# Kernel tuning notes

Hardware: AMD Instinct MI355X
Metric: run time of the kernel (lower is better)

## Reference

```python
import jax, jax.numpy as jnp
import numpy as np


def _ternarize(p, delta, w):
    # {-w, 0, +w} via threshold mask, matching TrainableTernarize.forward
    return jnp.where(p > delta, w, jnp.where(p < -delta, -w, jnp.zeros_like(p)))


def _ternary_para(p, w):
    # TrainableTernaryPara.forward: delta = 0.05 * max|p|
    delta = 0.05 * jnp.max(jnp.abs(p))
    return _ternarize(p, delta, w)


def _init_scale(p):
    # w init: mean(|p|[|p| > 0.7 * mean|p|])
    a = jnp.abs(p)
    mask = (a > 0.7 * jnp.mean(a)).astype(p.dtype)
    return jnp.sum(a * mask) / jnp.sum(mask)


def setup_inputs() -> dict:
    key = jax.random.key(0)
    k1, k2, k3 = jax.random.split(key, 3)
    B, S, D_IN, D_OUT = 4, 2048, 4096, 4096
    x = jax.random.normal(k1, (B, S, D_IN), dtype=jnp.float32)
    bound = 1.0 / np.sqrt(D_IN)  # nn.Linear default init range
    W = jax.random.uniform(k2, (D_OUT, D_IN), minval=-bound, maxval=bound, dtype=jnp.float32)
    b = jax.random.uniform(k3, (D_OUT,), minval=-bound, maxval=bound, dtype=jnp.float32)
    w_scale = _init_scale(W)
    b_scale = _init_scale(b)
    return {"x": x, "W": W, "w_scale": w_scale, "b": b, "b_scale": b_scale}


def reference(x, W, w_scale, b, b_scale):
    Wt = _ternary_para(W, w_scale)   # [D_OUT, D_IN] in {-w,0,+w}
    bt = _ternary_para(b, b_scale)   # [D_OUT]
    # F.linear(x, Wt, bt) = x @ Wt.T + bt
    return jnp.einsum('bsi,oi->bso', x, Wt) + bt
```

## Files before the change

kernel.cpp:

```cpp
#include <hip/hip_runtime.h>

typedef int v4i __attribute__((ext_vector_type(4)));
typedef int v16i __attribute__((ext_vector_type(16)));

#define BM 256
#define BN 256
#define BKB 64
#define NRING 4

#define GLOAD_LDS(gptr, lptr)                                                         \
  __builtin_amdgcn_global_load_lds(                                                   \
      (const __attribute__((address_space(1))) unsigned int*)(gptr),                  \
      (__attribute__((address_space(3))) unsigned int*)(lptr), 16, 0, 0)


__device__ __forceinline__ float max4abs(float4 v) {
  return fmaxf(fmaxf(fabsf(v.x), fabsf(v.y)), fmaxf(fabsf(v.z), fabsf(v.w)));
}

__device__ __forceinline__ int packq4(float4 v, float inv) {
  int b0 = ((int)fminf(127.f, fmaxf(-127.f, rintf(v.x * inv)))) & 255;
  int b1 = ((int)fminf(127.f, fmaxf(-127.f, rintf(v.y * inv)))) & 255;
  int b2 = ((int)fminf(127.f, fmaxf(-127.f, rintf(v.z * inv)))) & 255;
  int b3 = ((int)fminf(127.f, fmaxf(-127.f, rintf(v.w * inv)))) & 255;
  return b0 | (b1 << 8) | (b2 << 16) | (b3 << 24);
}

__global__ void prep1_kernel(const float4* __restrict__ X4,
                             signed char* __restrict__ Q,
                             float* __restrict__ sx, int K, int nrows,
                             const float4* __restrict__ W4, long nW4,
                             const float4* __restrict__ b4, int nb4,
                             unsigned* __restrict__ mx) {
  __shared__ float sm[4];
  const int tid = threadIdx.x;
  const int bid = blockIdx.x;

  if (bid < nrows) {
    const float4* xr = X4 + (size_t)bid * (K / 4);
    float4 v0 = xr[tid], v1 = xr[tid + 256], v2 = xr[tid + 512], v3 = xr[tid + 768];
    float m = fmaxf(fmaxf(max4abs(v0), max4abs(v1)), fmaxf(max4abs(v2), max4abs(v3)));
    for (int off = 32; off > 0; off >>= 1) m = fmaxf(m, __shfl_down(m, off));
    if ((tid & 63) == 0) sm[tid >> 6] = m;
    __syncthreads();
    const float total = fmaxf(fmaxf(sm[0], sm[1]), fmaxf(sm[2], sm[3]));
    const float inv = 127.f / total;
    int* qw = (int*)(Q + (size_t)bid * K);
    qw[tid]       = packq4(v0, inv);
    qw[tid + 256] = packq4(v1, inv);
    qw[tid + 512] = packq4(v2, inv);
    qw[tid + 768] = packq4(v3, inv);
    if (tid == 0) sx[bid] = total * (1.f / 127.f);
    return;
  }

  float m = 0.f;
  const bool isB = (bid == gridDim.x - 1);
  if (!isB) {
    const long wb = bid - nrows;
    const long stride = 1024L * blockDim.x;
    for (long i = wb * blockDim.x + tid; i < nW4; i += stride)
      m = fmaxf(m, max4abs(W4[i]));
  } else {
    for (int i = tid; i < nb4; i += blockDim.x) m = fmaxf(m, max4abs(b4[i]));
  }
  for (int off = 32; off > 0; off >>= 1) m = fmaxf(m, __shfl_down(m, off));
  if ((tid & 63) == 0) sm[tid >> 6] = m;
  __syncthreads();
  if (tid == 0) {
    m = fmaxf(fmaxf(sm[0], sm[1]), fmaxf(sm[2], sm[3]));
    atomicMax(mx + (isB ? 1 : 0), __float_as_uint(m));
  }
}

__global__ void prep_w_kernel(const float4* __restrict__ W4, long nW4,
                              const float4* __restrict__ b4, int nb4,
                              const unsigned* __restrict__ mx,
                              const float* __restrict__ bscale,
                              int* __restrict__ Twi, float4* __restrict__ bt) {
  if (blockIdx.x == gridDim.x - 1) {
    const float delta = 0.05f * __uint_as_float(mx[1]);
    const float s = *bscale;
    for (int i = threadIdx.x; i < nb4; i += blockDim.x) {
      float4 v = b4[i];
      float4 o;
      o.x = v.x > delta ? s : (v.x < -delta ? -s : 0.f);
      o.y = v.y > delta ? s : (v.y < -delta ? -s : 0.f);
      o.z = v.z > delta ? s : (v.z < -delta ? -s : 0.f);
      o.w = v.w > delta ? s : (v.w < -delta ? -s : 0.f);
      bt[i] = o;
    }
    return;
  }
  const float delta = 0.05f * __uint_as_float(mx[0]);
  const long stride = (long)(gridDim.x - 1) * blockDim.x;
  for (long i = blockIdx.x * (long)blockDim.x + threadIdx.x; i < nW4; i += stride) {
    float4 w = W4[i];
    int b0 = w.x > delta ? 1 : (w.x < -delta ? 0xFF : 0);
    int b1 = w.y > delta ? 1 : (w.y < -delta ? 0xFF : 0);
    int b2 = w.z > delta ? 1 : (w.z < -delta ? 0xFF : 0);
    int b3 = w.w > delta ? 1 : (w.w < -delta ? 0xFF : 0);
    Twi[i] = b0 | (b1 << 8) | (b2 << 16) | (b3 << 24);
  }
}

__global__ __launch_bounds__(512, 2) void gemm_tern_i8(
    const signed char* __restrict__ A,
    const signed char* __restrict__ B,
    const float* __restrict__ sx,
    const float* __restrict__ bt,
    const float* __restrict__ wsc,
    float* __restrict__ C,
    int M, int N, int K) {
  __shared__ __align__(16) signed char lds[NRING][2][BM * BKB];

  const int tid = threadIdx.x;
  const int wave = tid >> 6;
  const int lane = tid & 63;
  const int wm = wave >> 2, wn = wave & 3;
  const int l32 = lane & 31;
  const int khalf = lane >> 5;

  const unsigned orig = blockIdx.x;
  const unsigned xcd = orig & 7;
  const unsigned r8 = orig >> 3;
  const int by = (int)(xcd * 4 + (r8 & 3));
  const int bx = (int)(r8 >> 2);
  const int bm0 = by * BM;
  const int bn0 = bx * BN;

  const signed char* gA[2];
  const signed char* gB[2];
#pragma unroll
  for (int j = 0; j < 2; ++j) {
    const int idx = j * 512 + tid;
    const int row = idx >> 2;
    const int gch = (idx & 3) ^ ((idx >> 3) & 3);
    gA[j] = A + (size_t)(bm0 + row) * K + gch * 16;
    gB[j] = B + (size_t)(bn0 + row) * K + gch * 16;
  }
  const int ldsbase = wave * 64 * 16;

#define STAGE(slot)                                  \
  do {                                               \
    signed char* la = &lds[slot][0][ldsbase];        \
    signed char* lb = &lds[slot][1][ldsbase];        \
    GLOAD_LDS(gA[0], la);                            \
    GLOAD_LDS(gA[1], la + 8192);                     \
    GLOAD_LDS(gB[0], lb);                            \
    GLOAD_LDS(gB[1], lb + 8192);                     \
    gA[0] += BKB; gA[1] += BKB;                      \
    gB[0] += BKB; gB[1] += BKB;                      \
  } while (0)

  const int q = (l32 >> 1) & 3;
  const int pos0 = (khalf + 0) ^ q;
  const int pos1 = (khalf + 2) ^ q;
  const int aoff0 = (wm * 128 + l32) * BKB + pos0 * 16;
  const int aoff1 = (wm * 128 + l32) * BKB + pos1 * 16;
  const int boff0 = (wn * 64 + l32) * BKB + pos0 * 16;
  const int boff1 = (wn * 64 + l32) * BKB + pos1 * 16;

  v16i acc[4][2] = {};
  v4i bfA[2][2], bfB[2][2];

  const int NT = K / BKB;

  STAGE(0); STAGE(1); STAGE(2);
  asm volatile("s_waitcnt vmcnt(4)" ::: "memory");
  asm volatile("s_barrier" ::: "memory");

#pragma unroll
  for (int nt = 0; nt < 2; ++nt) {
    bfA[nt][0] = *(const v4i*)(&lds[0][1][0] + boff0 + nt * 2048);
    bfA[nt][1] = *(const v4i*)(&lds[0][1][0] + boff1 + nt * 2048);
  }

#define BODY(T, CUR, NXT)                                                              \
  do {                                                                                 \
    const int slot_ = (T) & 3;                                                         \
    if ((T) + 3 < NT) STAGE(((T) + 3) & 3);                                            \
    const signed char* sa_ = &lds[slot_][0][0];                                        \
    v4i af_[4][2];                                                                     \
    _Pragma("unroll")                                                                  \
    for (int mt = 0; mt < 4; ++mt) {                                                   \
      af_[mt][0] = *(const v4i*)(sa_ + aoff0 + mt * 2048);                             \
      af_[mt][1] = *(const v4i*)(sa_ + aoff1 + mt * 2048);                             \
    }                                                                                  \
    if ((T) + 1 < NT) {                                                                \
      const signed char* sbn_ = &lds[((T) + 1) & 3][1][0];                             \
      _Pragma("unroll")                                                                \
      for (int nt = 0; nt < 2; ++nt) {                                                 \
        NXT[nt][0] = *(const v4i*)(sbn_ + boff0 + nt * 2048);                          \
        NXT[nt][1] = *(const v4i*)(sbn_ + boff1 + nt * 2048);                          \
      }                                                                                \
    }                                                                                  \
    __builtin_amdgcn_s_setprio(1);                                                     \
    _Pragma("unroll")                                                                  \
    for (int mt = 0; mt < 4; ++mt)                                                     \
      _Pragma("unroll")                                                                \
      for (int nt = 0; nt < 2; ++nt) {                                                 \
        acc[mt][nt] = __builtin_amdgcn_mfma_i32_32x32x32_i8(af_[mt][0], CUR[nt][0],    \
                                                            acc[mt][nt], 0, 0, 0);    \
        acc[mt][nt] = __builtin_amdgcn_mfma_i32_32x32x32_i8(af_[mt][1], CUR[nt][1],    \
                                                            acc[mt][nt], 0, 0, 0);    \
      }                                                                                \
    __builtin_amdgcn_s_setprio(0);                                                     \
    asm volatile("s_waitcnt vmcnt(4)" ::: "memory");                                   \
    asm volatile("s_barrier" ::: "memory");                                            \
  } while (0)

  for (int t = 0; t < NT - 2; t += 2) {
    BODY(t, bfA, bfB);
    BODY(t + 1, bfB, bfA);
  }
  asm volatile("s_waitcnt vmcnt(0)" ::: "memory");
  asm volatile("s_barrier" ::: "memory");
  BODY(NT - 2, bfA, bfB);
  BODY(NT - 1, bfB, bfA);
#undef BODY
#undef STAGE

  const float ws = *wsc;
#pragma unroll
  for (int mt = 0; mt < 4; ++mt) {
    const int rowbase = bm0 + wm * 128 + mt * 32 + 4 * khalf;
#pragma unroll
    for (int nt = 0; nt < 2; ++nt) {
      const int col = bn0 + wn * 64 + nt * 32 + l32;
      const float bias = bt[col];
#pragma unroll
      for (int r = 0; r < 16; ++r) {
        const int row = rowbase + (r & 3) + 8 * (r >> 2);
        C[(size_t)row * N + col] = ws * sx[row] * (float)acc[mt][nt][r] + bias;
      }
    }
  }
}


extern "C" void kernel_launch(void* const* d_in, const int* in_sizes, int n_in,
                              void* d_out, int out_size, void* d_ws, size_t ws_size,
                              hipStream_t stream) {
  const float* x = (const float*)d_in[0];
  const float* W = (const float*)d_in[1];
  const float* w_scale = (const float*)d_in[2];
  const float* b = (const float*)d_in[3];
  const float* b_scale = (const float*)d_in[4];
  float* out = (float*)d_out;

  const int K = 4096;
  const int N = in_sizes[3];
  const int M = in_sizes[0] / K;

  char* ws = (char*)d_ws;
  signed char* xb = (signed char*)ws;
  signed char* Tw = (signed char*)(ws + (size_t)M * K);
  float* bt = (float*)(ws + (size_t)M * K + (size_t)N * K);
  float* sx = bt + N;
  unsigned* mx = (unsigned*)(sx + M);

  hipMemsetAsync(mx, 0, 8, stream);

  const long nW4 = (long)N * K / 4;
  const int nb4 = N / 4;

  prep1_kernel<<<M + 1024 + 1, 256, 0, stream>>>((const float4*)x, xb, sx, K, M,
                                                 (const float4*)W, nW4,
                                                 (const float4*)b, nb4, mx);

  prep_w_kernel<<<2049, 256, 0, stream>>>((const float4*)W, nW4,
                                          (const float4*)b, nb4, mx, b_scale,
                                          (int*)Tw, (float4*)bt);

  const int nwg = (N / BN) * (M / BM);
  gemm_tern_i8<<<nwg, 512, 0, stream>>>(xb, Tw, sx, bt, w_scale, out, M, N, K);
}
```

Measured before the change: 413.1 us.

## Shrink GEMM tile to 256x128 with 4 waves and 3-slot LDS ring

Changes the int8 GEMM block tile from 256x256 with 8 waves to 256x128 with 4 waves. The LDS ring drops from 4 to 3 stages, packed into one flat buffer, and the LDS swizzle is adjusted. The B-fragment prefetch across iterations is removed, so each step loads A and B fragments from the current slot. The intent is a smaller LDS footprint and more workgroups for better occupancy and load balance, at the cost of lower arithmetic intensity per tile and less latency hiding from the register double-buffering.

```diff
diff --git a/kernel.cpp b/kernel.cpp
--- a/kernel.cpp
+++ b/kernel.cpp
@@ -4,9 +4,10 @@
 typedef int v16i __attribute__((ext_vector_type(16)));
 
 #define BM 256
-#define BN 256
+#define BN 128
 #define BKB 64
-#define NRING 4
+#define SLOT (BM * BKB + BN * BKB)
+#define NRING 3
 
 #define GLOAD_LDS(gptr, lptr)                                                         \
   __builtin_amdgcn_global_load_lds(                                                   \
@@ -104,7 +105,7 @@
   }
 }
 
-__global__ __launch_bounds__(512, 2) void gemm_tern_i8(
+__global__ __launch_bounds__(256, 2) void gemm_tern_i8(
     const signed char* __restrict__ A,
     const signed char* __restrict__ B,
     const float* __restrict__ sx,
@@ -112,12 +113,12 @@
     const float* __restrict__ wsc,
     float* __restrict__ C,
     int M, int N, int K) {
-  __shared__ __align__(16) signed char lds[NRING][2][BM * BKB];
+  __shared__ __align__(16) signed char lds[NRING * SLOT];
 
   const int tid = threadIdx.x;
   const int wave = tid >> 6;
   const int lane = tid & 63;
-  const int wm = wave >> 2, wn = wave & 3;
+  const int wm = wave >> 1, wn = wave & 1;
   const int l32 = lane & 31;
   const int khalf = lane >> 5;
 
@@ -129,95 +130,90 @@
   const int bm0 = by * BM;
   const int bn0 = bx * BN;
 
-  const signed char* gA[2];
+  const signed char* gA[4];
   const signed char* gB[2];
 #pragma unroll
-  for (int j = 0; j < 2; ++j) {
-    const int idx = j * 512 + tid;
+  for (int j = 0; j < 4; ++j) {
+    const int idx = j * 256 + tid;
     const int row = idx >> 2;
-    const int gch = (idx & 3) ^ ((idx >> 3) & 3);
+    const int gch = (idx & 3) ^ ((idx >> 3) & 3) ^ (((idx >> 6) & 1) << 1);
     gA[j] = A + (size_t)(bm0 + row) * K + gch * 16;
-    gB[j] = B + (size_t)(bn0 + row) * K + gch * 16;
-  }
-  const int ldsbase = wave * 64 * 16;
-
-#define STAGE(slot)                                  \
+    if (j < 2) gB[j] = B + (size_t)(bn0 + row) * K + gch * 16;
+  }
+  const int wbase = wave * 1024;
+
+#define STAGE(wo)                                    \
   do {                                               \
-    signed char* la = &lds[slot][0][ldsbase];        \
-    signed char* lb = &lds[slot][1][ldsbase];        \
-    GLOAD_LDS(gA[0], la);                            \
-    GLOAD_LDS(gA[1], la + 8192);                     \
-    GLOAD_LDS(gB[0], lb);                            \
-    GLOAD_LDS(gB[1], lb + 8192);                     \
-    gA[0] += BKB; gA[1] += BKB;                      \
-    gB[0] += BKB; gB[1] += BKB;                      \
+    signed char* l = lds + (wo) + wbase;             \
+    GLOAD_LDS(gA[0], l);                             \
+    GLOAD_LDS(gA[1], l + 4096);                      \
+    GLOAD_LDS(gA[2], l + 8192);                      \
+    GLOAD_LDS(gA[3], l + 12288);                     \
+    GLOAD_LDS(gB[0], l + 16384);                     \
+    GLOAD_LDS(gB[1], l + 20480);                     \
+    gA[0] += BKB; gA[1] += BKB; gA[2] += BKB;        \
+    gA[3] += BKB; gB[0] += BKB; gB[1] += BKB;        \
   } while (0)
 
-  const int q = (l32 >> 1) & 3;
-  const int pos0 = (khalf + 0) ^ q;
-  const int pos1 = (khalf + 2) ^ q;
-  const int aoff0 = (wm * 128 + l32) * BKB + pos0 * 16;
-  const int aoff1 = (wm * 128 + l32) * BKB + pos1 * 16;
-  const int boff0 = (wn * 64 + l32) * BKB + pos0 * 16;
-  const int boff1 = (wn * 64 + l32) * BKB + pos1 * 16;
+  const int swzr = ((l32 >> 1) & 3) ^ (((l32 >> 4) & 1) << 1);
+  const int pos0 = khalf ^ swzr;
+  const int pos1 = pos0 ^ 2;
+  const int arow = (wm * 128 + l32) * BKB;
+  const int brow = BM * BKB + (wn * 64 + l32) * BKB;
+  const int aoff0 = arow + pos0 * 16, aoff1 = arow + pos1 * 16;
+  const int boff0 = brow + pos0 * 16, boff1 = brow + pos1 * 16;
 
   v16i acc[4][2] = {};
-  v4i bfA[2][2], bfB[2][2];
-
-  const int NT = K / BKB;
-
-  STAGE(0); STAGE(1); STAGE(2);
-  asm volatile("s_waitcnt vmcnt(4)" ::: "memory");
-  asm volatile("s_barrier" ::: "memory");
-
-#pragma unroll
-  for (int nt = 0; nt < 2; ++nt) {
-    bfA[nt][0] = *(const v4i*)(&lds[0][1][0] + boff0 + nt * 2048);
-    bfA[nt][1] = *(const v4i*)(&lds[0][1][0] + boff1 + nt * 2048);
-  }
-
-#define BODY(T, CUR, NXT)                                                              \
+
+#define BODY(ro)                                                                       \
   do {                                                                                 \
-    const int slot_ = (T) & 3;                                                         \
-    if ((T) + 3 < NT) STAGE(((T) + 3) & 3);                                            \
-    const signed char* sa_ = &lds[slot_][0][0];                                        \
-    v4i af_[4][2];                                                                     \
+    const signed char* s_ = lds + (ro);                                                \
+    v4i af_[4][2], bf_[2][2];                                                          \
     _Pragma("unroll")                                                                  \
     for (int mt = 0; mt < 4; ++mt) {                                                   \
-      af_[mt][0] = *(const v4i*)(sa_ + aoff0 + mt * 2048);                             \
-      af_[mt][1] = *(const v4i*)(sa_ + aoff1 + mt * 2048);                             \
+      af_[mt][0] = *(const v4i*)(s_ + aoff0 + mt * 2048);                              \
+      af_[mt][1] = *(const v4i*)(s_ + aoff1 + mt * 2048);                              \
     }                                                                                  \
-    if ((T) + 1 < NT) {                                                                \
-      const signed char* sbn_ = &lds[((T) + 1) & 3][1][0];                             \
-      _Pragma("unroll")                                                                \
-      for (int nt = 0; nt < 2; ++nt) {                                                 \
-        NXT[nt][0] = *(const v4i*)(sbn_ + boff0 + nt * 2048);                          \
-        NXT[nt][1] = *(const v4i*)(sbn_ + boff1 + nt * 2048);                          \
-      }                                                                                \
+    _Pragma("unroll")                                                                  \
+    for (int nt = 0; nt < 2; ++nt) {                                                   \
+      bf_[nt][0] = *(const v4i*)(s_ + boff0 + nt * 2048);                              \
+      bf_[nt][1] = *(const v4i*)(s_ + boff1 + nt * 2048);                              \
     }                                                                                  \
     __builtin_amdgcn_s_setprio(1);                                                     \
     _Pragma("unroll")                                                                  \
     for (int mt = 0; mt < 4; ++mt)                                                     \
       _Pragma("unroll")                                                                \
       for (int nt = 0; nt < 2; ++nt) {                                                 \
-        acc[mt][nt] = __builtin_amdgcn_mfma_i32_32x32x32_i8(af_[mt][0], CUR[nt][0],    \
+        acc[mt][nt] = __builtin_amdgcn_mfma_i32_32x32x32_i8(af_[mt][0], bf_[nt][0],    \
                                                             acc[mt][nt], 0, 0, 0);    \
-        acc[mt][nt] = __builtin_amdgcn_mfma_i32_32x32x32_i8(af_[mt][1], CUR[nt][1],    \
+        acc[mt][nt] = __builtin_amdgcn_mfma_i32_32x32x32_i8(af_[mt][1], bf_[nt][1],    \
                                                             acc[mt][nt], 0, 0, 0);    \
       }                                                                                \
     __builtin_amdgcn_s_setprio(0);                                                     \
-    asm volatile("s_waitcnt vmcnt(4)" ::: "memory");                                   \
-    asm volatile("s_barrier" ::: "memory");                                            \
   } while (0)
 
-  for (int t = 0; t < NT - 2; t += 2) {
-    BODY(t, bfA, bfB);
-    BODY(t + 1, bfB, bfA);
-  }
+  const int NT = K / BKB;
+
+  STAGE(0);
+  STAGE(SLOT);
+  asm volatile("s_waitcnt vmcnt(6)" ::: "memory");
+  asm volatile("s_barrier" ::: "memory");
+
+  int ro = 0;
+  int wo = 2 * SLOT;
+  for (int t = 0; t < NT - 2; ++t) {
+    STAGE(wo);
+    wo = (wo == 2 * SLOT) ? 0 : wo + SLOT;
+    BODY(ro);
+    asm volatile("s_waitcnt vmcnt(6)" ::: "memory");
+    asm volatile("s_barrier" ::: "memory");
+    ro = (ro == 2 * SLOT) ? 0 : ro + SLOT;
+  }
+  BODY(ro);
+  ro = (ro == 2 * SLOT) ? 0 : ro + SLOT;
   asm volatile("s_waitcnt vmcnt(0)" ::: "memory");
   asm volatile("s_barrier" ::: "memory");
-  BODY(NT - 2, bfA, bfB);
-  BODY(NT - 1, bfB, bfA);
+  BODY(ro);
 #undef BODY
 #undef STAGE
 
@@ -274,5 +270,5 @@
                                           (int*)Tw, (float4*)bt);
 
   const int nwg = (N / BN) * (M / BM);
-  gemm_tern_i8<<<nwg, 512, 0, stream>>>(xb, Tw, sx, bt, w_scale, out, M, N, K);
-}
+  gemm_tern_i8<<<nwg, 256, 0, stream>>>(xb, Tw, sx, bt, w_scale, out, M, N, K);
+}
```

Measured after the change: 417.6 us. Within noise of the previous version (+1.1%).
